# Optimization experiments

Hardware: AMD Instinct MI355X
Metric: run time of the kernel (lower is better)

Reference implementation:

```python
import jax, jax.numpy as jnp
import numpy as np

N = 10000
E = 640000
IN_F = 128
HID = 16
HEADS = 8
NEG_SLOPE = 0.2


def setup_inputs() -> dict:
    key = jax.random.key(0)
    ks = jax.random.split(key, 12)
    g = lambda k, shape: jax.random.normal(k, shape, dtype=jnp.float32) * (1.0 / np.sqrt(shape[0]))
    return {
        "x": jax.random.normal(ks[0], (N, IN_F), dtype=jnp.float32),
        "edge_index": jax.random.randint(ks[1], (2, E), 0, N, dtype=jnp.int32),
        "W1": g(ks[2], (IN_F, HEADS * HID)),
        "att_src1": jax.random.normal(ks[3], (HEADS, HID), dtype=jnp.float32) * 0.1,
        "att_dst1": jax.random.normal(ks[4], (HEADS, HID), dtype=jnp.float32) * 0.1,
        "b1": jnp.zeros((HEADS * HID,), dtype=jnp.float32),
        "W2": g(ks[5], (HEADS * HID, HEADS * HID)),
        "att_src2": jax.random.normal(ks[6], (HEADS, HID), dtype=jnp.float32) * 0.1,
        "att_dst2": jax.random.normal(ks[7], (HEADS, HID), dtype=jnp.float32) * 0.1,
        "b2": jnp.zeros((HID,), dtype=jnp.float32),
    }


def gat_layer(x, src, dst, W, a_src, a_dst, bias, concat):
    # x: [N, Fin]; src/dst: [E'] (self-loops already included)
    H, F = a_src.shape
    h = (x @ W).reshape(-1, H, F)                      # [N, H, F]
    # per-node attention terms, gathered per edge
    s_src = jnp.einsum('nhf,hf->nh', h, a_src)          # [N, H]
    s_dst = jnp.einsum('nhf,hf->nh', h, a_dst)          # [N, H]
    e = s_src[src] + s_dst[dst]                         # [E', H]
    e = jnp.where(e >= 0, e, NEG_SLOPE * e)             # LeakyReLU(0.2)
    # segment softmax over incoming edges of each dst node
    m = jax.ops.segment_max(e, dst, num_segments=N)     # [N, H]
    ex = jnp.exp(e - m[dst])
    denom = jax.ops.segment_sum(ex, dst, num_segments=N)
    alpha = ex / denom[dst]                             # [E', H]
    out = jax.ops.segment_sum(alpha[:, :, None] * h[src], dst, num_segments=N)  # [N, H, F]
    out = out.reshape(-1, H * F) if concat else out.mean(axis=1)
    return out + bias


def reference(x, edge_index, W1, att_src1, att_dst1, b1, W2, att_src2, att_dst2, b2):
    loops = jnp.arange(N, dtype=edge_index.dtype)
    src = jnp.concatenate([edge_index[0], loops])
    dst = jnp.concatenate([edge_index[1], loops])
    h = gat_layer(x, src, dst, W1, att_src1, att_dst1, b1, concat=True)
    h = jax.nn.relu(h)
    out = gat_layer(h, src, dst, W2, att_src2, att_dst2, b2, concat=False)
    return out
```

## Files before the change

kernel.cpp:

```cpp
#include <hip/hip_runtime.h>
#include <math.h>

#define N_NODES 10000
#define E_EDGES 640000
#define EP_EDGES (E_EDGES + N_NODES)
#define HEADS 8
#define NEG_SLOPE 0.2f

static __device__ __forceinline__ float leaky(float x){ return x >= 0.f ? x : NEG_SLOPE * x; }

__global__ __launch_bounds__(256) void k_zero(int* __restrict__ p, int n){
  int i = blockIdx.x * 256 + threadIdx.x;
  if (i < n) p[i] = 0;
}

__global__ __launch_bounds__(256) void k_hist(const int* __restrict__ ei, int* __restrict__ deg){
  int e = blockIdx.x * 256 + threadIdx.x;
  if (e >= EP_EDGES) return;
  int dst = (e < E_EDGES) ? ei[E_EDGES + e] : (e - E_EDGES);
  atomicAdd(&deg[dst], 1);
}

__global__ __launch_bounds__(1024) void k_scan(const int* __restrict__ deg,
                                               int* __restrict__ off,
                                               int* __restrict__ cur){
  __shared__ int wsum[16];
  int t = threadIdx.x, lane = t & 63, w = t >> 6;
  if (t == 0) off[0] = 0;
  int carry = 0;
  for (int base = 0; base < N_NODES; base += 1024){
    int i = base + t;
    int v = (i < N_NODES) ? deg[i] : 0;
    int x = v;
    #pragma unroll
    for (int o = 1; o < 64; o <<= 1){
      int y = __shfl_up(x, o);
      if (lane >= o) x += y;
    }
    if (lane == 63) wsum[w] = x;
    __syncthreads();
    int wpre = 0, tot = 0;
    #pragma unroll
    for (int j = 0; j < 16; ++j){ int s = wsum[j]; if (j < w) wpre += s; tot += s; }
    int inc = carry + wpre + x;
    if (i < N_NODES){ off[i + 1] = inc; cur[i] = inc - v; }
    carry += tot;
    __syncthreads();
  }
}

__global__ __launch_bounds__(256) void k_scatter(const int* __restrict__ ei,
                                                 int* __restrict__ cur,
                                                 int* __restrict__ csr){
  int e = blockIdx.x * 256 + threadIdx.x;
  if (e >= EP_EDGES) return;
  int src, dst;
  if (e < E_EDGES){ src = ei[e]; dst = ei[E_EDGES + e]; }
  else            { src = dst = e - E_EDGES; }
  int pos = atomicAdd(&cur[dst], 1);
  csr[pos] = src;
}

__global__ __launch_bounds__(256) void k_gemm(const float* __restrict__ X,
                                              const float* __restrict__ W,
                                              float* __restrict__ Y, int nrows){
  __shared__ float ws[128 * 128];
  __shared__ float xs[32][129];
  int t = threadIdx.x;
  {
    const float4* W4 = (const float4*)W;
    float4* ws4 = (float4*)ws;
    #pragma unroll 4
    for (int i = t; i < 4096; i += 256) ws4[i] = W4[i];
  }
  int row0 = blockIdx.x * 32;
  for (int i = t; i < 32 * 128; i += 256){
    int r = i >> 7, k = i & 127;
    float v = (row0 + r < nrows) ? X[(size_t)(row0 + r) * 128 + k] : 0.f;
    xs[r][k] = v;
  }
  __syncthreads();
  int r0 = (t >> 5) * 4;
  int c0 = (t & 31) * 4;
  float acc[4][4];
  #pragma unroll
  for (int i = 0; i < 4; ++i)
    #pragma unroll
    for (int j = 0; j < 4; ++j) acc[i][j] = 0.f;
  #pragma unroll 8
  for (int k = 0; k < 128; ++k){
    float4 wv = *(const float4*)&ws[k * 128 + c0];
    float x0 = xs[r0 + 0][k], x1 = xs[r0 + 1][k], x2 = xs[r0 + 2][k], x3 = xs[r0 + 3][k];
    acc[0][0] += x0 * wv.x; acc[0][1] += x0 * wv.y; acc[0][2] += x0 * wv.z; acc[0][3] += x0 * wv.w;
    acc[1][0] += x1 * wv.x; acc[1][1] += x1 * wv.y; acc[1][2] += x1 * wv.z; acc[1][3] += x1 * wv.w;
    acc[2][0] += x2 * wv.x; acc[2][1] += x2 * wv.y; acc[2][2] += x2 * wv.z; acc[2][3] += x2 * wv.w;
    acc[3][0] += x3 * wv.x; acc[3][1] += x3 * wv.y; acc[3][2] += x3 * wv.z; acc[3][3] += x3 * wv.w;
  }
  #pragma unroll
  for (int i = 0; i < 4; ++i){
    int r = row0 + r0 + i;
    if (r < nrows)
      *(float4*)&Y[(size_t)r * 128 + c0] = make_float4(acc[i][0], acc[i][1], acc[i][2], acc[i][3]);
  }
}

__global__ __launch_bounds__(256) void k_scores(const float* __restrict__ H,
    const float* __restrict__ a_src, const float* __restrict__ a_dst,
    float* __restrict__ s_src, float* __restrict__ s_dst){
  int idx = blockIdx.x * 256 + threadIdx.x;
  if (idx >= N_NODES * HEADS) return;
  int n = idx >> 3, h = idx & 7;
  const float* hp = H + (size_t)n * 128 + h * 16;
  const float* as = a_src + h * 16;
  const float* ad = a_dst + h * 16;
  float s1 = 0.f, s2 = 0.f;
  #pragma unroll
  for (int f = 0; f < 16; ++f){ float v = hp[f]; s1 += v * as[f]; s2 += v * ad[f]; }
  s_src[idx] = s1;
  s_dst[idx] = s2;
}

template<int MODE>
__global__ __launch_bounds__(256) void k_agg(const float* __restrict__ H,
    const float* __restrict__ s_src, const float* __restrict__ s_dst,
    const int* __restrict__ csr, const int* __restrict__ off,
    const float* __restrict__ bias, float* __restrict__ out){
  int wave = (blockIdx.x * 256 + threadIdx.x) >> 6;
  int lane = threadIdx.x & 63;
  if (wave >= N_NODES) return;
  int n = __builtin_amdgcn_readfirstlane(wave);
  int beg = off[n], end = off[n + 1];

  float sdst[HEADS];
  #pragma unroll
  for (int h = 0; h < HEADS; ++h) sdst[h] = s_dst[n * 8 + h];

  float m[HEADS], ssum[HEADS];
  #pragma unroll
  for (int h = 0; h < HEADS; ++h){ m[h] = -1e30f; ssum[h] = 0.f; }
  for (int i = beg + lane; i < end; i += 64){
    int s = csr[i];
    const float* sp = s_src + s * 8;
    #pragma unroll
    for (int h = 0; h < HEADS; ++h){
      float l = leaky(sp[h] + sdst[h]);
      float mn = fmaxf(m[h], l);
      ssum[h] = ssum[h] * __expf(m[h] - mn) + __expf(l - mn);
      m[h] = mn;
    }
  }
  #pragma unroll
  for (int h = 0; h < HEADS; ++h){
    #pragma unroll
    for (int o = 32; o; o >>= 1){
      float mo = __shfl_xor(m[h], o);
      float so = __shfl_xor(ssum[h], o);
      float mn = fmaxf(m[h], mo);
      ssum[h] = ssum[h] * __expf(m[h] - mn) + so * __expf(mo - mn);
      m[h] = mn;
    }
  }

  int g = lane >> 4;
  float mA = g == 0 ? m[0] : g == 1 ? m[1] : g == 2 ? m[2] : m[3];
  float sA = g == 0 ? ssum[0] : g == 1 ? ssum[1] : g == 2 ? ssum[2] : ssum[3];
  float dA = g == 0 ? sdst[0] : g == 1 ? sdst[1] : g == 2 ? sdst[2] : sdst[3];
  float mB = g == 0 ? m[4] : g == 1 ? m[5] : g == 2 ? m[6] : m[7];
  float sB = g == 0 ? ssum[4] : g == 1 ? ssum[5] : g == 2 ? ssum[6] : ssum[7];
  float dB = g == 0 ? sdst[4] : g == 1 ? sdst[5] : g == 2 ? sdst[6] : sdst[7];
  float invA = 1.f / sA, invB = 1.f / sB;

  float acc0 = 0.f, acc1 = 0.f;
  #pragma unroll 2
  for (int i = beg; i < end; ++i){
    int s = csr[i];
    const float* hp = H + (size_t)s * 128;
    float sa = s_src[s * 8 + g];
    float sb = s_src[s * 8 + 4 + g];
    float a0 = __expf(leaky(sa + dA) - mA) * invA;
    float a1 = __expf(leaky(sb + dB) - mB) * invB;
    acc0 += a0 * hp[lane];
    acc1 += a1 * hp[64 + lane];
  }

  if (MODE == 0){
    float v0 = acc0 + bias[lane];
    float v1 = acc1 + bias[64 + lane];
    out[(size_t)n * 128 + lane]      = fmaxf(v0, 0.f);
    out[(size_t)n * 128 + 64 + lane] = fmaxf(v1, 0.f);
  } else {
    float s2 = acc0 + acc1;
    s2 += __shfl_xor(s2, 16);
    s2 += __shfl_xor(s2, 32);
    if (lane < 16) out[(size_t)n * 16 + lane] = s2 * 0.125f + bias[lane];
  }
}

extern "C" void kernel_launch(void* const* d_in, const int* in_sizes, int n_in,
                              void* d_out, int out_size, void* d_ws, size_t ws_size,
                              hipStream_t stream){
  const float* x   = (const float*)d_in[0];
  const int*   ei  = (const int*)d_in[1];
  const float* W1  = (const float*)d_in[2];
  const float* as1 = (const float*)d_in[3];
  const float* ad1 = (const float*)d_in[4];
  const float* b1  = (const float*)d_in[5];
  const float* W2  = (const float*)d_in[6];
  const float* as2 = (const float*)d_in[7];
  const float* ad2 = (const float*)d_in[8];
  const float* b2  = (const float*)d_in[9];
  float* out = (float*)d_out;

  char* p = (char*)d_ws;
  auto alloc = [&](size_t bytes)->char*{
    char* r = p; p += (bytes + 255) & ~(size_t)255; return r;
  };
  int*   deg = (int*)  alloc((size_t)N_NODES * 4);
  int*   off = (int*)  alloc((size_t)(N_NODES + 1) * 4);
  int*   cur = (int*)  alloc((size_t)N_NODES * 4);
  int*   csr = (int*)  alloc((size_t)EP_EDGES * 4);
  float* h1  = (float*)alloc((size_t)N_NODES * 128 * 4);
  float* a1  = (float*)alloc((size_t)N_NODES * 128 * 4);
  float* ss1 = (float*)alloc((size_t)N_NODES * 8 * 4);
  float* sd1 = (float*)alloc((size_t)N_NODES * 8 * 4);
  float* ss2 = (float*)alloc((size_t)N_NODES * 8 * 4);
  float* sd2 = (float*)alloc((size_t)N_NODES * 8 * 4);
  float* h2  = h1;

  k_zero<<<(N_NODES + 255) / 256, 256, 0, stream>>>(deg, N_NODES);
  k_hist<<<(EP_EDGES + 255) / 256, 256, 0, stream>>>(ei, deg);
  k_scan<<<1, 1024, 0, stream>>>(deg, off, cur);
  k_scatter<<<(EP_EDGES + 255) / 256, 256, 0, stream>>>(ei, cur, csr);

  k_gemm<<<(N_NODES + 31) / 32, 256, 0, stream>>>(x, W1, h1, N_NODES);
  k_scores<<<(N_NODES * HEADS + 255) / 256, 256, 0, stream>>>(h1, as1, ad1, ss1, sd1);
  k_agg<0><<<(N_NODES + 3) / 4, 256, 0, stream>>>(h1, ss1, sd1, csr, off, b1, a1);

  k_gemm<<<(N_NODES + 31) / 32, 256, 0, stream>>>(a1, W2, h2, N_NODES);
  k_scores<<<(N_NODES * HEADS + 255) / 256, 256, 0, stream>>>(h2, as2, ad2, ss2, sd2);
  k_agg<1><<<(N_NODES + 3) / 4, 256, 0, stream>>>(h2, ss2, sd2, csr, off, b2, out);
}
```

Measured before the change: 321.3 us.

## Split each node's aggregation across two waves; drop GEMM weight staging in LDS

The aggregation kernel now gives each destination node two waves instead of one. Each wave handles four heads (64 features), which halves the per-wave serial edge loop and doubles parallelism. Layer 2 combines the two half-sums through shared memory. The GEMM no longer copies the 64KB weight matrix into LDS and reads it from global memory/cache instead, with float4 loads for X. This cuts LDS use and raises occupancy. k_zero is replaced by hipMemsetAsync. The costs are duplicated softmax-statistic work per node and an extra block sync in mode 1.

Result: faster. 298.9 us (-7.0%).

```diff
diff --git a/kernel.cpp b/kernel.cpp
--- a/kernel.cpp
+++ b/kernel.cpp
@@ -8,11 +8,6 @@
 #define NEG_SLOPE 0.2f
 
 static __device__ __forceinline__ float leaky(float x){ return x >= 0.f ? x : NEG_SLOPE * x; }
-
-__global__ __launch_bounds__(256) void k_zero(int* __restrict__ p, int n){
-  int i = blockIdx.x * 256 + threadIdx.x;
-  if (i < n) p[i] = 0;
-}
 
 __global__ __launch_bounds__(256) void k_hist(const int* __restrict__ ei, int* __restrict__ deg){
   int e = blockIdx.x * 256 + threadIdx.x;
@@ -64,20 +59,16 @@
 __global__ __launch_bounds__(256) void k_gemm(const float* __restrict__ X,
                                               const float* __restrict__ W,
                                               float* __restrict__ Y, int nrows){
-  __shared__ float ws[128 * 128];
   __shared__ float xs[32][129];
   int t = threadIdx.x;
-  {
-    const float4* W4 = (const float4*)W;
-    float4* ws4 = (float4*)ws;
-    #pragma unroll 4
-    for (int i = t; i < 4096; i += 256) ws4[i] = W4[i];
-  }
   int row0 = blockIdx.x * 32;
-  for (int i = t; i < 32 * 128; i += 256){
-    int r = i >> 7, k = i & 127;
-    float v = (row0 + r < nrows) ? X[(size_t)(row0 + r) * 128 + k] : 0.f;
-    xs[r][k] = v;
+  const float4* X4 = (const float4*)X;
+  for (int i = t; i < 1024; i += 256){
+    int r = i >> 5, k4 = i & 31;
+    float4 v = make_float4(0.f, 0.f, 0.f, 0.f);
+    if (row0 + r < nrows) v = X4[(size_t)(row0 + r) * 32 + k4];
+    xs[r][k4 * 4 + 0] = v.x; xs[r][k4 * 4 + 1] = v.y;
+    xs[r][k4 * 4 + 2] = v.z; xs[r][k4 * 4 + 3] = v.w;
   }
   __syncthreads();
   int r0 = (t >> 5) * 4;
@@ -87,9 +78,10 @@
   for (int i = 0; i < 4; ++i)
     #pragma unroll
     for (int j = 0; j < 4; ++j) acc[i][j] = 0.f;
+  const float4* W4 = (const float4*)W + (c0 >> 2);
   #pragma unroll 8
   for (int k = 0; k < 128; ++k){
-    float4 wv = *(const float4*)&ws[k * 128 + c0];
+    float4 wv = W4[(size_t)k * 32];
     float x0 = xs[r0 + 0][k], x1 = xs[r0 + 1][k], x2 = xs[r0 + 2][k], x3 = xs[r0 + 3][k];
     acc[0][0] += x0 * wv.x; acc[0][1] += x0 * wv.y; acc[0][2] += x0 * wv.z; acc[0][3] += x0 * wv.w;
     acc[1][0] += x1 * wv.x; acc[1][1] += x1 * wv.y; acc[1][2] += x1 * wv.z; acc[1][3] += x1 * wv.w;
@@ -125,74 +117,72 @@
     const float* __restrict__ s_src, const float* __restrict__ s_dst,
     const int* __restrict__ csr, const int* __restrict__ off,
     const float* __restrict__ bias, float* __restrict__ out){
-  int wave = (blockIdx.x * 256 + threadIdx.x) >> 6;
-  int lane = threadIdx.x & 63;
-  if (wave >= N_NODES) return;
-  int n = __builtin_amdgcn_readfirstlane(wave);
+  int t = threadIdx.x;
+  int lane = t & 63;
+  int wb = t >> 6;
+  int n = __builtin_amdgcn_readfirstlane(blockIdx.x * 2 + (wb >> 1));
+  int w = __builtin_amdgcn_readfirstlane(wb & 1);
+  int hbase = w * 4;
   int beg = off[n], end = off[n + 1];
 
-  float sdst[HEADS];
-  #pragma unroll
-  for (int h = 0; h < HEADS; ++h) sdst[h] = s_dst[n * 8 + h];
-
-  float m[HEADS], ssum[HEADS];
-  #pragma unroll
-  for (int h = 0; h < HEADS; ++h){ m[h] = -1e30f; ssum[h] = 0.f; }
+  float sdst[4];
+  #pragma unroll
+  for (int j = 0; j < 4; ++j) sdst[j] = s_dst[n * 8 + hbase + j];
+
+  float m[4], ssum[4];
+  #pragma unroll
+  for (int j = 0; j < 4; ++j){ m[j] = -1e30f; ssum[j] = 0.f; }
   for (int i = beg + lane; i < end; i += 64){
     int s = csr[i];
-    const float* sp = s_src + s * 8;
-    #pragma unroll
-    for (int h = 0; h < HEADS; ++h){
-      float l = leaky(sp[h] + sdst[h]);
-      float mn = fmaxf(m[h], l);
-      ssum[h] = ssum[h] * __expf(m[h] - mn) + __expf(l - mn);
-      m[h] = mn;
+    const float* sp = s_src + s * 8 + hbase;
+    #pragma unroll
+    for (int j = 0; j < 4; ++j){
+      float l = leaky(sp[j] + sdst[j]);
+      float mn = fmaxf(m[j], l);
+      ssum[j] = ssum[j] * __expf(m[j] - mn) + __expf(l - mn);
+      m[j] = mn;
     }
   }
   #pragma unroll
-  for (int h = 0; h < HEADS; ++h){
+  for (int j = 0; j < 4; ++j){
     #pragma unroll
     for (int o = 32; o; o >>= 1){
-      float mo = __shfl_xor(m[h], o);
-      float so = __shfl_xor(ssum[h], o);
-      float mn = fmaxf(m[h], mo);
-      ssum[h] = ssum[h] * __expf(m[h] - mn) + so * __expf(mo - mn);
-      m[h] = mn;
+      float mo = __shfl_xor(m[j], o);
+      float so = __shfl_xor(ssum[j], o);
+      float mn = fmaxf(m[j], mo);
+      ssum[j] = ssum[j] * __expf(m[j] - mn) + so * __expf(mo - mn);
+      m[j] = mn;
     }
   }
 
-  int g = lane >> 4;
-  float mA = g == 0 ? m[0] : g == 1 ? m[1] : g == 2 ? m[2] : m[3];
-  float sA = g == 0 ? ssum[0] : g == 1 ? ssum[1] : g == 2 ? ssum[2] : ssum[3];
-  float dA = g == 0 ? sdst[0] : g == 1 ? sdst[1] : g == 2 ? sdst[2] : sdst[3];
-  float mB = g == 0 ? m[4] : g == 1 ? m[5] : g == 2 ? m[6] : m[7];
-  float sB = g == 0 ? ssum[4] : g == 1 ? ssum[5] : g == 2 ? ssum[6] : ssum[7];
-  float dB = g == 0 ? sdst[4] : g == 1 ? sdst[5] : g == 2 ? sdst[6] : sdst[7];
-  float invA = 1.f / sA, invB = 1.f / sB;
-
-  float acc0 = 0.f, acc1 = 0.f;
-  #pragma unroll 2
+  int hl = lane >> 4;
+  float mA = hl == 0 ? m[0] : hl == 1 ? m[1] : hl == 2 ? m[2] : m[3];
+  float sA = hl == 0 ? ssum[0] : hl == 1 ? ssum[1] : hl == 2 ? ssum[2] : ssum[3];
+  float dA = hl == 0 ? sdst[0] : hl == 1 ? sdst[1] : hl == 2 ? sdst[2] : sdst[3];
+  float inv = 1.f / sA;
+
+  const float* Hw = H + 64 * w;
+  float acc = 0.f;
+  #pragma unroll 4
   for (int i = beg; i < end; ++i){
     int s = csr[i];
-    const float* hp = H + (size_t)s * 128;
-    float sa = s_src[s * 8 + g];
-    float sb = s_src[s * 8 + 4 + g];
-    float a0 = __expf(leaky(sa + dA) - mA) * invA;
-    float a1 = __expf(leaky(sb + dB) - mB) * invB;
-    acc0 += a0 * hp[lane];
-    acc1 += a1 * hp[64 + lane];
+    float sa = s_src[s * 8 + hbase + hl];
+    float a = __expf(leaky(sa + dA) - mA) * inv;
+    acc = fmaf(a, Hw[(size_t)s * 128 + lane], acc);
   }
 
   if (MODE == 0){
-    float v0 = acc0 + bias[lane];
-    float v1 = acc1 + bias[64 + lane];
-    out[(size_t)n * 128 + lane]      = fmaxf(v0, 0.f);
-    out[(size_t)n * 128 + 64 + lane] = fmaxf(v1, 0.f);
+    int f = 64 * w + lane;
+    out[(size_t)n * 128 + f] = fmaxf(acc + bias[f], 0.f);
   } else {
-    float s2 = acc0 + acc1;
+    float s2 = acc;
     s2 += __shfl_xor(s2, 16);
     s2 += __shfl_xor(s2, 32);
-    if (lane < 16) out[(size_t)n * 16 + lane] = s2 * 0.125f + bias[lane];
+    __shared__ float red[4][16];
+    if (lane < 16) red[wb][lane] = s2;
+    __syncthreads();
+    if ((wb & 1) == 0 && lane < 16)
+      out[(size_t)n * 16 + lane] = (red[wb][lane] + red[wb + 1][lane]) * 0.125f + bias[lane];
   }
 }
 
@@ -227,16 +217,16 @@
   float* sd2 = (float*)alloc((size_t)N_NODES * 8 * 4);
   float* h2  = h1;
 
-  k_zero<<<(N_NODES + 255) / 256, 256, 0, stream>>>(deg, N_NODES);
+  hipMemsetAsync(deg, 0, (size_t)N_NODES * 4, stream);
   k_hist<<<(EP_EDGES + 255) / 256, 256, 0, stream>>>(ei, deg);
   k_scan<<<1, 1024, 0, stream>>>(deg, off, cur);
   k_scatter<<<(EP_EDGES + 255) / 256, 256, 0, stream>>>(ei, cur, csr);
 
   k_gemm<<<(N_NODES + 31) / 32, 256, 0, stream>>>(x, W1, h1, N_NODES);
   k_scores<<<(N_NODES * HEADS + 255) / 256, 256, 0, stream>>>(h1, as1, ad1, ss1, sd1);
-  k_agg<0><<<(N_NODES + 3) / 4, 256, 0, stream>>>(h1, ss1, sd1, csr, off, b1, a1);
+  k_agg<0><<<N_NODES / 2, 256, 0, stream>>>(h1, ss1, sd1, csr, off, b1, a1);
 
   k_gemm<<<(N_NODES + 31) / 32, 256, 0, stream>>>(a1, W2, h2, N_NODES);
   k_scores<<<(N_NODES * HEADS + 255) / 256, 256, 0, stream>>>(h2, as2, ad2, ss2, sd2);
-  k_agg<1><<<(N_NODES + 3) / 4, 256, 0, stream>>>(h2, ss2, sd2, csr, off, b2, out);
-}
+  k_agg<1><<<N_NODES / 2, 256, 0, stream>>>(h2, ss2, sd2, csr, off, b2, out);
+}
```
